# Kernel tuning notes

Hardware: AMD Instinct MI355X
Metric: run time of the kernel (lower is better)

## Reference

```python
import jax, jax.numpy as jnp
import numpy as np

B, L, D = 4, 2048, 1024
H = 16
HD = D // H  # head_dim = 64
BASE = 10000.0


def rope_cos_sin(seq_len, head_dim, dtype=jnp.float32):
    inv_freq = 1.0 / (BASE ** (jnp.arange(0, head_dim, 2, dtype=jnp.float32) / head_dim))
    t = jnp.arange(seq_len, dtype=jnp.float32)
    freqs = jnp.outer(t, inv_freq)  # [L, HD/2]
    return jnp.cos(freqs).astype(dtype), jnp.sin(freqs).astype(dtype)


def apply_rope(x, cos, sin):
    # x: [B, H, L, HD]; cos/sin: [L, HD/2]
    x1 = x[..., ::2]
    x2 = x[..., 1::2]
    c = cos[None, None, :, :]
    s = sin[None, None, :, :]
    # NOTE: original concatenates halves (does not re-interleave)
    return jnp.concatenate([x1 * c - x2 * s, x1 * s + x2 * c], axis=-1)


def setup_inputs() -> dict:
    key = jax.random.key(0)
    k1, k2, k3 = jax.random.split(key, 3)
    x = jax.random.normal(k1, (B, L, D), dtype=jnp.float32)
    W_qkv = jax.random.normal(k2, (3 * D, D), dtype=jnp.float32) * (D ** -0.5)
    W_proj = jax.random.normal(k3, (D, D), dtype=jnp.float32) * (D ** -0.5)
    return {"x": x, "W_qkv": W_qkv, "W_proj": W_proj}


def reference(x, W_qkv, W_proj):
    b, l, d = x.shape
    scale = HD ** -0.5
    qkv = jnp.einsum('bld,ed->ble', x, W_qkv)            # [B, L, 3D]
    qkv = qkv.reshape(b, l, 3, H, HD)
    q, k, v = (jnp.transpose(qkv[:, :, i], (0, 2, 1, 3)) for i in range(3))  # [B,H,L,HD]
    cos, sin = rope_cos_sin(l, HD, x.dtype)
    q = apply_rope(q, cos, sin)
    k = apply_rope(k, cos, sin)
    attn = jnp.einsum('bhqd,bhkd->bhqk', q, k) * scale   # [B,H,L,L]
    attn = jax.nn.softmax(attn, axis=-1)
    out = jnp.einsum('bhqk,bhkd->bhqd', attn, v)         # [B,H,L,HD]
    out = jnp.transpose(out, (0, 2, 1, 3)).reshape(b, l, d)
    return jnp.einsum('bld,ed->ble', out, W_proj)
```

## Files before the change

### kernel.cpp

```cpp
#include <hip/hip_runtime.h>
#include <hip/hip_bf16.h>

typedef unsigned short u16;
typedef unsigned int u32;
typedef __attribute__((ext_vector_type(8))) short bf16x8;
typedef __attribute__((ext_vector_type(4))) float f32x4;
typedef __attribute__((ext_vector_type(2))) unsigned int u32x2;

#define NL 2048
#define NH 16

__device__ __forceinline__ float bf2f(u16 v) {
    union { float f; unsigned u; } x; x.u = ((unsigned)v) << 16; return x.f;
}
__device__ __forceinline__ u16 f2bf(float f) {
    union { __hip_bfloat16 h; u16 u; } x; x.h = __float2bfloat16(f); return x.u;
}
__device__ __forceinline__ u32 pk2(float a, float b) {
    union { float f; u32 u; } x, y; x.f = a; y.f = b;
    return ((x.u + 0x8000u) >> 16) | ((y.u + 0x8000u) & 0xffff0000u);
}
__device__ __forceinline__ u32 pkt(float lo, float hi) {
    union { float f; u32 u; } x, y; x.f = lo; y.f = hi;
    return __builtin_amdgcn_perm(y.u, x.u, 0x07060302u);
}
#if __has_builtin(__builtin_amdgcn_exp2f)
#define EXP2F(x) __builtin_amdgcn_exp2f(x)
#else
#define EXP2F(x) __expf((x) * 0.69314718056f)
#endif

__device__ __forceinline__ void quad_xchg(u32& a, u32& b) {
#if __has_builtin(__builtin_amdgcn_permlane32_swap) && __has_builtin(__builtin_amdgcn_permlane16_swap)
    u32x2 r0 = __builtin_amdgcn_permlane32_swap(a, b, false, false);
    u32x2 r1 = __builtin_amdgcn_permlane16_swap(r0.x, r0.y, false, false);
    a = r1.x; b = r1.y;
#else
    asm volatile("s_nop 1\n\t"
                 "v_permlane32_swap_b32 %0, %1\n\t"
                 "s_nop 1\n\t"
                 "v_permlane16_swap_b32 %0, %1\n\t"
                 "s_nop 1"
                 : "+v"(a), "+v"(b));
#endif
}

__device__ __forceinline__ void gload_lds16(const u16* g, u16* l) {
    __builtin_amdgcn_global_load_lds(
        (__attribute__((address_space(1))) void*)(g),
        (__attribute__((address_space(3))) void*)(l), 16, 0, 0);
}

__global__ __launch_bounds__(256) void cast_all_k(const float* __restrict__ x,
                                                  const float* __restrict__ wq,
                                                  const float* __restrict__ wp,
                                                  u16* __restrict__ xo,
                                                  u16* __restrict__ wqo,
                                                  u16* __restrict__ wpo,
                                                  float* __restrict__ cosT,
                                                  float* __restrict__ sinT) {
    if (blockIdx.x < 256) {
        int idx = blockIdx.x * 256 + threadIdx.x;
        int l = idx >> 5, i = idx & 31;
        float invf = exp2f(-(float)i * 0.41524101186092029f);
        float ang = (float)l * invf;
        cosT[idx] = cosf(ang);
        sinT[idx] = sinf(ang);
    }
    int i = blockIdx.x * 256 + threadIdx.x;
    const float* src; u16* dst; int off;
    if (i < 2097152)      { src = x;  dst = xo;  off = i; }
    else if (i < 2883584) { src = wq; dst = wqo; off = i - 2097152; }
    else                  { src = wp; dst = wpo; off = i - 2883584; }
    float4 v = *(const float4*)&src[(size_t)off * 4];
    u16 tmp[4] = {f2bf(v.x), f2bf(v.y), f2bf(v.z), f2bf(v.w)};
    *(ushort4*)&dst[(size_t)off * 4] = *(ushort4*)tmp;
}

template <typename OutT>
__global__ __launch_bounds__(256) void gemm_bt(const u16* __restrict__ A,
                                               const u16* __restrict__ Bm,
                                               OutT* __restrict__ C,
                                               int M, int N, int K) {
    __shared__ u16 As[128][64];
    __shared__ u16 Bs[128][64];
    const int t = threadIdx.x;
    const int lane = t & 63, wave = t >> 6;
    const int quad = lane >> 4, lrow = lane & 15;
    const int wr = wave >> 1, wc = wave & 1;
    const size_t m0 = (size_t)blockIdx.y * 128, n0 = (size_t)blockIdx.x * 128;

    const int srow = wave * 32 + (lane >> 3);
    const int scg  = (lane & 7) ^ (lane >> 3);

    f32x4 acc[4][4];
#pragma unroll
    for (int i = 0; i < 4; ++i)
#pragma unroll
        for (int j = 0; j < 4; ++j) acc[i][j] = (f32x4)0.0f;

    for (int k0 = 0; k0 < K; k0 += 64) {
#pragma unroll
        for (int j = 0; j < 4; ++j) {
            gload_lds16(&A[(m0 + srow + j * 8) * K + k0 + scg * 8],
                        &As[wave * 32 + j * 8][0]);
            gload_lds16(&Bm[(n0 + srow + j * 8) * K + k0 + scg * 8],
                        &Bs[wave * 32 + j * 8][0]);
        }
        __syncthreads();
#pragma unroll
        for (int ks = 0; ks < 2; ++ks) {
            bf16x8 av[4], bv[4];
#pragma unroll
            for (int i = 0; i < 4; ++i)
                av[i] = *(const bf16x8*)
                    &As[wr * 64 + i * 16 + lrow][(((ks << 2) | quad) ^ (lrow & 7)) << 3];
#pragma unroll
            for (int j = 0; j < 4; ++j)
                bv[j] = *(const bf16x8*)
                    &Bs[wc * 64 + j * 16 + lrow][(((ks << 2) | quad) ^ (lrow & 7)) << 3];
#pragma unroll
            for (int i = 0; i < 4; ++i)
#pragma unroll
                for (int j = 0; j < 4; ++j)
                    acc[i][j] = __builtin_amdgcn_mfma_f32_16x16x32_bf16(
                        av[i], bv[j], acc[i][j], 0, 0, 0);
        }
        __syncthreads();
    }
#pragma unroll
    for (int i = 0; i < 4; ++i)
#pragma unroll
        for (int r = 0; r < 4; ++r) {
            size_t row = m0 + wr * 64 + i * 16 + quad * 4 + r;
#pragma unroll
            for (int j = 0; j < 4; ++j) {
                size_t col = n0 + wc * 64 + j * 16 + lrow;
                if constexpr (sizeof(OutT) == 4)
                    C[row * N + col] = acc[i][j][r];
                else
                    C[row * N + col] = f2bf(acc[i][j][r]);
            }
        }
}

__global__ __launch_bounds__(512, 2) void gemm256_bt(const u16* __restrict__ A,
                                                     const u16* __restrict__ Bm,
                                                     u16* __restrict__ C,
                                                     int M, int N, int K) {
    __shared__ __align__(16) char smem[131072];
    const int t = threadIdx.x;
    const int lane = t & 63, w = t >> 6;
    const int quad = lane >> 4, lq = lane & 15;
    const int wm = w >> 2, wn = w & 3;
    const int rsub = lane >> 3;
    const int scg  = (lane & 7) ^ rsub;
    const size_t m0 = (size_t)blockIdx.y * 256, n0 = (size_t)blockIdx.x * 256;
    const int NT = K >> 6;

#define ASB(buf) ((u16(*)[64])(smem + (size_t)(buf) * 65536))
#define BSB(buf) ((u16(*)[64])(smem + (size_t)(buf) * 65536 + 32768))
#define STAGE_A(buf, half, kt) { \
    const size_t kro_ = (size_t)(kt) * 64 + (size_t)(scg * 8); \
    gload_lds16(&A[(m0 + (half) * 128 + w * 16 + 0 + rsub) * (size_t)K + kro_], \
                &ASB(buf)[(half) * 128 + w * 16 + 0][0]); \
    gload_lds16(&A[(m0 + (half) * 128 + w * 16 + 8 + rsub) * (size_t)K + kro_], \
                &ASB(buf)[(half) * 128 + w * 16 + 8][0]); }
#define STAGE_B(buf, half, kt) { \
    const size_t kro_ = (size_t)(kt) * 64 + (size_t)(scg * 8); \
    gload_lds16(&Bm[(n0 + (half) * 128 + w * 16 + 0 + rsub) * (size_t)K + kro_], \
                &BSB(buf)[(half) * 128 + w * 16 + 0][0]); \
    gload_lds16(&Bm[(n0 + (half) * 128 + w * 16 + 8 + rsub) * (size_t)K + kro_], \
                &BSB(buf)[(half) * 128 + w * 16 + 8][0]); }
#define RD_A(dst, rowbase) { \
    _Pragma("unroll") for (int m_ = 0; m_ < 4; ++m_) \
    _Pragma("unroll") for (int ks_ = 0; ks_ < 2; ++ks_) \
        dst[m_][ks_] = *(const bf16x8*) \
            &Ac[(rowbase) + m_ * 16 + lq][(((ks_ << 2) | quad) ^ (lq & 7)) << 3]; }
#define RD_B(dst, rowbase) { \
    _Pragma("unroll") for (int n_ = 0; n_ < 2; ++n_) \
    _Pragma("unroll") for (int ks_ = 0; ks_ < 2; ++ks_) \
        dst[n_][ks_] = *(const bf16x8*) \
            &Bc[(rowbase) + n_ * 16 + lq][(((ks_ << 2) | quad) ^ (lq & 7)) << 3]; }
#define MM(QM, QN, bvv) { \
    _Pragma("unroll") for (int m_ = 0; m_ < 4; ++m_) \
    _Pragma("unroll") for (int n_ = 0; n_ < 2; ++n_) \
    _Pragma("unroll") for (int ks_ = 0; ks_ < 2; ++ks_) \
        acc[QM][QN][m_][n_] = __builtin_amdgcn_mfma_f32_16x16x32_bf16( \
            av[m_][ks_], bvv[n_][ks_], acc[QM][QN][m_][n_], 0, 0, 0); }

    f32x4 acc[2][2][4][2];
#pragma unroll
    for (int a = 0; a < 2; ++a)
#pragma unroll
        for (int b = 0; b < 2; ++b)
#pragma unroll
            for (int m = 0; m < 4; ++m)
#pragma unroll
                for (int n = 0; n < 2; ++n) acc[a][b][m][n] = (f32x4)0.0f;
    bf16x8 av[4][2], bv0[2][2], bv1[2][2];

    STAGE_A(0, 0, 0); STAGE_B(0, 0, 0); STAGE_B(0, 1, 0); STAGE_A(0, 1, 0);
    asm volatile("s_waitcnt vmcnt(4)" ::: "memory");
    __builtin_amdgcn_s_barrier();

    for (int kt = 0; kt < NT - 1; ++kt) {
        const int cur = kt & 1, nxt = cur ^ 1;
        u16 (*Ac)[64] = ASB(cur);
        u16 (*Bc)[64] = BSB(cur);

        RD_A(av, wm * 64);
        RD_B(bv0, wn * 32);
        STAGE_A(nxt, 0, kt + 1);
        __builtin_amdgcn_s_barrier();
        __builtin_amdgcn_s_setprio(1);
        MM(0, 0, bv0);
        __builtin_amdgcn_s_setprio(0);
        asm volatile("s_waitcnt vmcnt(4)" ::: "memory");
        __builtin_amdgcn_s_barrier();

        RD_B(bv1, 128 + wn * 32);
        STAGE_B(nxt, 0, kt + 1);
        __builtin_amdgcn_s_barrier();
        __builtin_amdgcn_s_setprio(1);
        MM(0, 1, bv1);
        __builtin_amdgcn_s_setprio(0);
        asm volatile("s_waitcnt vmcnt(4)" ::: "memory");
        __builtin_amdgcn_s_barrier();

        RD_A(av, 128 + wm * 64);
        STAGE_B(nxt, 1, kt + 1);
        __builtin_amdgcn_s_barrier();
        __builtin_amdgcn_s_setprio(1);
        MM(1, 1, bv1);
        __builtin_amdgcn_s_setprio(0);
        __builtin_amdgcn_s_barrier();

        RD_B(bv0, wn * 32);
        STAGE_A(nxt, 1, kt + 1);
        __builtin_amdgcn_s_barrier();
        __builtin_amdgcn_s_setprio(1);
        MM(1, 0, bv0);
        __builtin_amdgcn_s_setprio(0);
        asm volatile("s_waitcnt vmcnt(4)" ::: "memory");
        __builtin_amdgcn_s_barrier();
    }

    {
        u16 (*Ac)[64] = ASB((NT - 1) & 1);
        u16 (*Bc)[64] = BSB((NT - 1) & 1);
        RD_A(av, wm * 64);
        RD_B(bv0, wn * 32);
        MM(0, 0, bv0);
        asm volatile("s_waitcnt vmcnt(2)" ::: "memory");
        __builtin_amdgcn_s_barrier();
        RD_B(bv1, 128 + wn * 32);
        MM(0, 1, bv1);
        asm volatile("s_waitcnt vmcnt(0)" ::: "memory");
        __builtin_amdgcn_s_barrier();
        RD_A(av, 128 + wm * 64);
        MM(1, 1, bv1);
        MM(1, 0, bv0);
    }

#pragma unroll
    for (int QM = 0; QM < 2; ++QM)
#pragma unroll
        for (int QN = 0; QN < 2; ++QN)
#pragma unroll
            for (int m = 0; m < 4; ++m)
#pragma unroll
                for (int r = 0; r < 4; ++r) {
                    size_t row = m0 + QM * 128 + wm * 64 + m * 16 + quad * 4 + r;
#pragma unroll
                    for (int n = 0; n < 2; ++n) {
                        size_t col = n0 + QN * 128 + wn * 32 + n * 16 + lq;
                        C[row * N + col] = f2bf(acc[QM][QN][m][n][r]);
                    }
                }
#undef ASB
#undef BSB
#undef STAGE_A
#undef STAGE_B
#undef RD_A
#undef RD_B
#undef MM
}

__global__ __launch_bounds__(256) void rope_vt_k(const u16* __restrict__ qkv,
                                                 const float* __restrict__ cosT,
                                                 const float* __restrict__ sinT,
                                                 u16* __restrict__ Q,
                                                 u16* __restrict__ Ko,
                                                 u16* __restrict__ VT) {
    __shared__ u16 vtile[64][72];
    const int lt = blockIdx.x, bh = blockIdx.y;
    const int b = bh >> 4, h = bh & 15;
    const int l0 = lt * 64;
    const int t = threadIdx.x;
    const float SC = 0.180336879f;
#pragma unroll
    for (int c = 0; c < 2; ++c) {
        int flat8 = c * 256 + t;
        int li = flat8 >> 3, dg = flat8 & 7;
        const u16* rowp = qkv + (size_t)(b * NL + l0 + li) * 3072 + h * 64 + dg * 8;
        uint4 qv = *(const uint4*)rowp;
        uint4 kv = *(const uint4*)(rowp + 1024);
        uint4 vv = *(const uint4*)(rowp + 2048);
        *(uint4*)&vtile[li][dg * 8] = vv;
        float4 cs = *(const float4*)&cosT[(l0 + li) * 32 + dg * 4];
        float4 sn = *(const float4*)&sinT[(l0 + li) * 32 + dg * 4];
        union { float f; u32 u; } w;
        float e0, o0, e1, o1, e2, o2, e3, o3;
        w.u = qv.x << 16; e0 = w.f; w.u = qv.x & 0xffff0000u; o0 = w.f;
        w.u = qv.y << 16; e1 = w.f; w.u = qv.y & 0xffff0000u; o1 = w.f;
        w.u = qv.z << 16; e2 = w.f; w.u = qv.z & 0xffff0000u; o2 = w.f;
        w.u = qv.w << 16; e3 = w.f; w.u = qv.w & 0xffff0000u; o3 = w.f;
        float c0 = cs.x * SC, c1 = cs.y * SC, c2 = cs.z * SC, c3 = cs.w * SC;
        float s0 = sn.x * SC, s1 = sn.y * SC, s2 = sn.z * SC, s3 = sn.w * SC;
        size_t ob = ((size_t)(b * NH + h) * NL + l0 + li) * 64;
        *(uint2*)&Q[ob + dg * 4] =
            make_uint2(pk2(e0 * c0 - o0 * s0, e1 * c1 - o1 * s1),
                       pk2(e2 * c2 - o2 * s2, e3 * c3 - o3 * s3));
        *(uint2*)&Q[ob + 32 + dg * 4] =
            make_uint2(pk2(e0 * s0 + o0 * c0, e1 * s1 + o1 * c1),
                       pk2(e2 * s2 + o2 * c2, e3 * s3 + o3 * c3));
        float f0, g0, f1, g1, f2, g2, f3, g3;
        w.u = kv.x << 16; f0 = w.f; w.u = kv.x & 0xffff0000u; g0 = w.f;
        w.u = kv.y << 16; f1 = w.f; w.u = kv.y & 0xffff0000u; g1 = w.f;
        w.u = kv.z << 16; f2 = w.f; w.u = kv.z & 0xffff0000u; g2 = w.f;
        w.u = kv.w << 16; f3 = w.f; w.u = kv.w & 0xffff0000u; g3 = w.f;
        *(uint2*)&Ko[ob + dg * 4] =
            make_uint2(pk2(f0 * cs.x - g0 * sn.x, f1 * cs.y - g1 * sn.y),
                       pk2(f2 * cs.z - g2 * sn.z, f3 * cs.w - g3 * sn.w));
        *(uint2*)&Ko[ob + 32 + dg * 4] =
            make_uint2(pk2(f0 * sn.x + g0 * cs.x, f1 * sn.y + g1 * cs.y),
                       pk2(f2 * sn.z + g2 * cs.z, f3 * sn.w + g3 * cs.w));
    }
    __syncthreads();
#pragma unroll
    for (int c = 0; c < 2; ++c) {
        int flat8 = c * 256 + t;
        int d = flat8 >> 3, lg = flat8 & 7;
        u16 tmp[8];
#pragma unroll
        for (int e = 0; e < 8; ++e) tmp[e] = vtile[lg * 8 + e][d];
        *(uint4*)&VT[((size_t)(bh * 64 + d)) * NL + l0 + lg * 8] = *(uint4*)tmp;
    }
}

__global__ __launch_bounds__(512, 4) void attn_k(const u16* __restrict__ Q,
                                                 const u16* __restrict__ Kg,
                                                 const u16* __restrict__ VT,
                                                 u16* __restrict__ Og) {
    __shared__ __align__(16) char smem[65536];
    u16 (*KsB)[64][64] = (u16(*)[64][64])(smem);
    u16 (*VsB)[64][64] = (u16(*)[64][64])(smem + 16384);
    const int t = threadIdx.x;
    const int lane = t & 63, wave = t >> 6;
    const int quad = lane >> 4, lq = lane & 15;

    const int flat = blockIdx.y * 8 + blockIdx.x;
    const int qt = (flat >> 3) & 7;
    const int bh = (flat & 7) + ((flat >> 6) << 3);
    const int q0 = qt * 256;
    const size_t qkbase = (size_t)bh * NL * 64;

    const int rsub = lane >> 3;
    const int scg  = (lane & 7) ^ rsub;

    u16 (*Qtmp)[64] = (u16(*)[64])(smem + 32768);
#pragma unroll
    for (int j = 0; j < 4; ++j)
        gload_lds16(&Q[qkbase + (size_t)(q0 + wave * 32 + j * 8 + rsub) * 64 + scg * 8],
                    &Qtmp[wave * 32 + j * 8][0]);
    const u16* kptr = Kg + qkbase + (size_t)(wave * 8 + rsub) * 64 + scg * 8;
    const u16* vptr = VT + qkbase + (size_t)(wave * 8 + rsub) * NL + scg * 8;
    gload_lds16(kptr, &KsB[0][wave * 8][0]);
    gload_lds16(vptr, &VsB[0][wave * 8][0]);
    kptr += 64 * 64;
    vptr += 64;
    __syncthreads();
    bf16x8 bq[2][2];
#pragma unroll
    for (int qh = 0; qh < 2; ++qh)
#pragma unroll
        for (int ks = 0; ks < 2; ++ks)
            bq[qh][ks] = *(const bf16x8*)
                &Qtmp[wave * 32 + qh * 16 + lq][(((ks << 2) | quad) ^ (lq & 7)) << 3];

    const bf16x8 ones = (bf16x8)(short)16256;
    f32x4 ot[2][4];
#pragma unroll
    for (int qh = 0; qh < 2; ++qh)
#pragma unroll
        for (int mt = 0; mt < 4; ++mt) ot[qh][mt] = (f32x4)0.0f;
    f32x4 lacc[2] = {(f32x4)0.0f, (f32x4)0.0f};

    for (int kc = 0; kc < NL / 64; ++kc) {
        __syncthreads();
        if (kc < NL / 64 - 1) {
            gload_lds16(kptr, &KsB[(kc + 1) & 1][wave * 8][0]);
            gload_lds16(vptr, &VsB[(kc + 1) & 1][wave * 8][0]);
            kptr += 64 * 64;
            vptr += 64;
        }
        const int cur = kc & 1;

        f32x4 st[2][4];
#pragma unroll
        for (int qh = 0; qh < 2; ++qh)
#pragma unroll
            for (int mt = 0; mt < 4; ++mt) st[qh][mt] = (f32x4)0.0f;
#pragma unroll
        for (int half = 0; half < 2; ++half)
#pragma unroll
            for (int ks = 0; ks < 2; ++ks)
#pragma unroll
                for (int m2 = 0; m2 < 2; ++m2) {
                    const int mt = half * 2 + m2;
                    bf16x8 ak = *(const bf16x8*)
                        &KsB[cur][mt * 16 + lq][(((ks << 2) | quad) ^ (lq & 7)) << 3];
                    st[0][mt] = __builtin_amdgcn_mfma_f32_16x16x32_bf16(ak, bq[0][ks], st[0][mt], 0, 0, 0);
                    st[1][mt] = __builtin_amdgcn_mfma_f32_16x16x32_bf16(ak, bq[1][ks], st[1][mt], 0, 0, 0);
                }

#pragma unroll
        for (int ks = 0; ks < 2; ++ks) {
            bf16x8 av[4];
#pragma unroll
            for (int mt = 0; mt < 4; ++mt)
                av[mt] = *(const bf16x8*)
                    &VsB[cur][mt * 16 + lq][(((ks << 2) | quad) ^ (lq & 7)) << 3];

            bf16x8 bp[2];
#pragma unroll
            for (int qh = 0; qh < 2; ++qh) {
                u32 a0, b0, a1, b1;
                {
                    const int mt = 2 * ks;
                    a0 = pkt(EXP2F(st[qh][mt][0]), EXP2F(st[qh][mt][1]));
                    a1 = pkt(EXP2F(st[qh][mt][2]), EXP2F(st[qh][mt][3]));
                }
                {
                    const int mt = 2 * ks + 1;
                    b0 = pkt(EXP2F(st[qh][mt][0]), EXP2F(st[qh][mt][1]));
                    b1 = pkt(EXP2F(st[qh][mt][2]), EXP2F(st[qh][mt][3]));
                }
                quad_xchg(a0, b0);
                quad_xchg(a1, b1);
                union { u32 u[4]; bf16x8 v; } bb;
                bb.u[0] = a0;
                bb.u[1] = a1;
                bb.u[2] = b0;
                bb.u[3] = b1;
                bp[qh] = bb.v;
            }

            lacc[0] = __builtin_amdgcn_mfma_f32_16x16x32_bf16(ones, bp[0], lacc[0], 0, 0, 0);
            lacc[1] = __builtin_amdgcn_mfma_f32_16x16x32_bf16(ones, bp[1], lacc[1], 0, 0, 0);
#pragma unroll
            for (int mt = 0; mt < 4; ++mt) {
                ot[0][mt] = __builtin_amdgcn_mfma_f32_16x16x32_bf16(av[mt], bp[0], ot[0][mt], 0, 0, 0);
                ot[1][mt] = __builtin_amdgcn_mfma_f32_16x16x32_bf16(av[mt], bp[1], ot[1][mt], 0, 0, 0);
            }
        }
    }

    __syncthreads();
    float* OT_ls = (float*)(smem + wave * 4352);
    float* Ls_ls = (float*)(smem + 34816);
    const int b = bh >> 4, h = bh & 15;
    const int qq = lane >> 2, dblk = lane & 3;
#pragma unroll
    for (int qh = 0; qh < 2; ++qh) {
#pragma unroll
        for (int mt = 0; mt < 4; ++mt)
#pragma unroll
            for (int r = 0; r < 4; ++r)
                OT_ls[(mt * 16 + quad * 4 + r) * 17 + lq] = ot[qh][mt][r];
        if (quad == 0) Ls_ls[wave * 16 + lq] = lacc[qh][0];
        __builtin_amdgcn_s_waitcnt(0xc07f);

        float rls = 1.0f / Ls_ls[wave * 16 + qq];
        u16 tmp[16];
#pragma unroll
        for (int e = 0; e < 16; ++e)
            tmp[e] = f2bf(OT_ls[(dblk * 16 + e) * 17 + qq] * rls);
        size_t orow = (size_t)b * NL + q0 + wave * 32 + qh * 16 + qq;
        size_t obase = orow * 1024 + h * 64 + dblk * 16;
        *(uint4*)&Og[obase] = *(uint4*)&tmp[0];
        *(uint4*)&Og[obase + 8] = *(uint4*)&tmp[8];
    }
}

extern "C" void kernel_launch(void* const* d_in, const int* in_sizes, int n_in,
                              void* d_out, int out_size, void* d_ws, size_t ws_size,
                              hipStream_t stream) {
    const float* x     = (const float*)d_in[0];
    const float* Wqkv  = (const float*)d_in[1];
    const float* Wproj = (const float*)d_in[2];
    float* out = (float*)d_out;

    char* ws = (char*)d_ws;
    u16* qkv     = (u16*)ws;
    u16* attnout = (u16*)ws;
    u16* Qw      = (u16*)(ws + 50331648);
    u16* Kw      = (u16*)(ws + 67108864);
    u16* VTw     = (u16*)(ws + 83886080);
    float* cosT  = (float*)(ws + 100663296);
    float* sinT  = (float*)(ws + 100925440);
    u16* x_bf    = (u16*)(ws + 101187584);
    u16* Wqkv_bf = (u16*)(ws + 117964800);
    u16* Wproj_bf= (u16*)(ws + 124256256);

    cast_all_k<<<12288, 256, 0, stream>>>(x, Wqkv, Wproj, x_bf, Wqkv_bf, Wproj_bf,
                                          cosT, sinT);
    gemm256_bt<<<dim3(12, 32), 512, 0, stream>>>(x_bf, Wqkv_bf, qkv, 8192, 3072, 1024);
    rope_vt_k<<<dim3(32, 64), 256, 0, stream>>>(qkv, cosT, sinT, Qw, Kw, VTw);
    attn_k<<<dim3(8, 64), 512, 0, stream>>>(Qw, Kw, VTw, attnout);
    gemm_bt<float><<<dim3(8, 64), 256, 0, stream>>>(attnout, Wproj_bf, out, 8192, 1024, 1024);
}
```

Baseline: 270.1 us.

## Fuse RoPE, scaling and V transpose into the QKV GEMM epilogue

The QKV projection GEMM now writes Q and K directly in head-major layout with RoPE and the softmax scale applied, and writes V transposed. Neighbouring even/odd columns are paired with a lane shuffle. This removes the separate rope_vt_k kernel and the round trip of the bf16 qkv intermediate through global memory. In exchange the epilogue does scattered 2-byte stores with per-element cos/sin loads, which may coalesce poorly, and the cos/sin tables are packed into one float2 table.

```diff
diff --git a/kernel.cpp b/kernel.cpp
--- a/kernel.cpp
+++ b/kernel.cpp
@@ -10,15 +10,8 @@
 #define NL 2048
 #define NH 16
 
-__device__ __forceinline__ float bf2f(u16 v) {
-    union { float f; unsigned u; } x; x.u = ((unsigned)v) << 16; return x.f;
-}
 __device__ __forceinline__ u16 f2bf(float f) {
     union { __hip_bfloat16 h; u16 u; } x; x.h = __float2bfloat16(f); return x.u;
-}
-__device__ __forceinline__ u32 pk2(float a, float b) {
-    union { float f; u32 u; } x, y; x.f = a; y.f = b;
-    return ((x.u + 0x8000u) >> 16) | ((y.u + 0x8000u) & 0xffff0000u);
 }
 __device__ __forceinline__ u32 pkt(float lo, float hi) {
     union { float f; u32 u; } x, y; x.f = lo; y.f = hi;
@@ -57,15 +50,13 @@
                                                   u16* __restrict__ xo,
                                                   u16* __restrict__ wqo,
                                                   u16* __restrict__ wpo,
-                                                  float* __restrict__ cosT,
-                                                  float* __restrict__ sinT) {
+                                                  float2* __restrict__ cs2T) {
     if (blockIdx.x < 256) {
         int idx = blockIdx.x * 256 + threadIdx.x;
         int l = idx >> 5, i = idx & 31;
         float invf = exp2f(-(float)i * 0.41524101186092029f);
         float ang = (float)l * invf;
-        cosT[idx] = cosf(ang);
-        sinT[idx] = sinf(ang);
+        cs2T[idx] = make_float2(cosf(ang), sinf(ang));
     }
     int i = blockIdx.x * 256 + threadIdx.x;
     const float* src; u16* dst; int off;
@@ -144,10 +135,13 @@
         }
 }
 
-__global__ __launch_bounds__(512, 2) void gemm256_bt(const u16* __restrict__ A,
-                                                     const u16* __restrict__ Bm,
-                                                     u16* __restrict__ C,
-                                                     int M, int N, int K) {
+__global__ __launch_bounds__(512, 2) void gemm256_qkv(const u16* __restrict__ A,
+                                                      const u16* __restrict__ Bm,
+                                                      u16* __restrict__ Qo,
+                                                      u16* __restrict__ Ko,
+                                                      u16* __restrict__ VTo,
+                                                      const float2* __restrict__ cs2T,
+                                                      int M, int K) {
     __shared__ __align__(16) char smem[131072];
     const int t = threadIdx.x;
     const int lane = t & 63, w = t >> 6;
@@ -263,21 +257,64 @@
         MM(1, 0, bv0);
     }
 
-#pragma unroll
-    for (int QM = 0; QM < 2; ++QM)
+    const int sect = (int)(n0 >> 10);
+    const int colb = (int)(n0 & 1023);
+    if (sect < 2) {
+        u16* __restrict__ outp = sect ? Ko : Qo;
+        const float sc = sect ? 1.0f : 0.180336879f;
+        const int odd = lq & 1;
 #pragma unroll
         for (int QN = 0; QN < 2; ++QN)
 #pragma unroll
-            for (int m = 0; m < 4; ++m)
-#pragma unroll
-                for (int r = 0; r < 4; ++r) {
-                    size_t row = m0 + QM * 128 + wm * 64 + m * 16 + quad * 4 + r;
-#pragma unroll
-                    for (int n = 0; n < 2; ++n) {
-                        size_t col = n0 + QN * 128 + wn * 32 + n * 16 + lq;
-                        C[row * N + col] = f2bf(acc[QM][QN][m][n][r]);
+            for (int n = 0; n < 2; ++n) {
+                const int col = colb + QN * 128 + wn * 32 + n * 16 + lq;
+                const int h = col >> 6;
+                const int d2 = (col & 63) >> 1;
+                const int dim = d2 + 32 * odd;
+#pragma unroll
+                for (int QM = 0; QM < 2; ++QM)
+#pragma unroll
+                    for (int m = 0; m < 4; ++m) {
+                        const size_t row = m0 + QM * 128 + wm * 64 + m * 16 + quad * 4;
+                        const int l0 = (int)(row & 2047);
+                        const int b = (int)(row >> 11);
+                        const size_t ob = ((size_t)(b * 16 + h) * 2048 + l0) * 64 + dim;
+#pragma unroll
+                        for (int r = 0; r < 4; ++r) {
+                            float v = acc[QM][QN][m][n][r];
+                            float pv = __shfl_xor(v, 1, 64);
+                            float2 cs = cs2T[(l0 + r) * 32 + d2];
+                            float c = cs.x * sc, s = cs.y * sc;
+                            float outv = odd ? (pv * s + v * c)
+                                             : (v * c - pv * s);
+                            outp[ob + (size_t)r * 64] = f2bf(outv);
+                        }
                     }
-                }
+            }
+    } else {
+#pragma unroll
+        for (int QN = 0; QN < 2; ++QN)
+#pragma unroll
+            for (int n = 0; n < 2; ++n) {
+                const int col = colb + QN * 128 + wn * 32 + n * 16 + lq;
+                const int h = col >> 6;
+                const int d = col & 63;
+#pragma unroll
+                for (int QM = 0; QM < 2; ++QM)
+#pragma unroll
+                    for (int m = 0; m < 4; ++m) {
+                        const size_t row = m0 + QM * 128 + wm * 64 + m * 16 + quad * 4;
+                        const int l0 = (int)(row & 2047);
+                        const int b = (int)(row >> 11);
+                        u16 t4[4];
+#pragma unroll
+                        for (int r = 0; r < 4; ++r)
+                            t4[r] = f2bf(acc[QM][QN][m][n][r]);
+                        *(uint2*)&VTo[((size_t)((b * 16 + h) * 64 + d)) * 2048 + l0] =
+                            *(uint2*)t4;
+                    }
+            }
+    }
 #undef ASB
 #undef BSB
 #undef STAGE_A
@@ -285,68 +322,6 @@
 #undef RD_A
 #undef RD_B
 #undef MM
-}
-
-__global__ __launch_bounds__(256) void rope_vt_k(const u16* __restrict__ qkv,
-                                                 const float* __restrict__ cosT,
-                                                 const float* __restrict__ sinT,
-                                                 u16* __restrict__ Q,
-                                                 u16* __restrict__ Ko,
-                                                 u16* __restrict__ VT) {
-    __shared__ u16 vtile[64][72];
-    const int lt = blockIdx.x, bh = blockIdx.y;
-    const int b = bh >> 4, h = bh & 15;
-    const int l0 = lt * 64;
-    const int t = threadIdx.x;
-    const float SC = 0.180336879f;
-#pragma unroll
-    for (int c = 0; c < 2; ++c) {
-        int flat8 = c * 256 + t;
-        int li = flat8 >> 3, dg = flat8 & 7;
-        const u16* rowp = qkv + (size_t)(b * NL + l0 + li) * 3072 + h * 64 + dg * 8;
-        uint4 qv = *(const uint4*)rowp;
-        uint4 kv = *(const uint4*)(rowp + 1024);
-        uint4 vv = *(const uint4*)(rowp + 2048);
-        *(uint4*)&vtile[li][dg * 8] = vv;
-        float4 cs = *(const float4*)&cosT[(l0 + li) * 32 + dg * 4];
-        float4 sn = *(const float4*)&sinT[(l0 + li) * 32 + dg * 4];
-        union { float f; u32 u; } w;
-        float e0, o0, e1, o1, e2, o2, e3, o3;
-        w.u = qv.x << 16; e0 = w.f; w.u = qv.x & 0xffff0000u; o0 = w.f;
-        w.u = qv.y << 16; e1 = w.f; w.u = qv.y & 0xffff0000u; o1 = w.f;
-        w.u = qv.z << 16; e2 = w.f; w.u = qv.z & 0xffff0000u; o2 = w.f;
-        w.u = qv.w << 16; e3 = w.f; w.u = qv.w & 0xffff0000u; o3 = w.f;
-        float c0 = cs.x * SC, c1 = cs.y * SC, c2 = cs.z * SC, c3 = cs.w * SC;
-        float s0 = sn.x * SC, s1 = sn.y * SC, s2 = sn.z * SC, s3 = sn.w * SC;
-        size_t ob = ((size_t)(b * NH + h) * NL + l0 + li) * 64;
-        *(uint2*)&Q[ob + dg * 4] =
-            make_uint2(pk2(e0 * c0 - o0 * s0, e1 * c1 - o1 * s1),
-                       pk2(e2 * c2 - o2 * s2, e3 * c3 - o3 * s3));
-        *(uint2*)&Q[ob + 32 + dg * 4] =
-            make_uint2(pk2(e0 * s0 + o0 * c0, e1 * s1 + o1 * c1),
-                       pk2(e2 * s2 + o2 * c2, e3 * s3 + o3 * c3));
-        float f0, g0, f1, g1, f2, g2, f3, g3;
-        w.u = kv.x << 16; f0 = w.f; w.u = kv.x & 0xffff0000u; g0 = w.f;
-        w.u = kv.y << 16; f1 = w.f; w.u = kv.y & 0xffff0000u; g1 = w.f;
-        w.u = kv.z << 16; f2 = w.f; w.u = kv.z & 0xffff0000u; g2 = w.f;
-        w.u = kv.w << 16; f3 = w.f; w.u = kv.w & 0xffff0000u; g3 = w.f;
-        *(uint2*)&Ko[ob + dg * 4] =
-            make_uint2(pk2(f0 * cs.x - g0 * sn.x, f1 * cs.y - g1 * sn.y),
-                       pk2(f2 * cs.z - g2 * sn.z, f3 * cs.w - g3 * sn.w));
-        *(uint2*)&Ko[ob + 32 + dg * 4] =
-            make_uint2(pk2(f0 * sn.x + g0 * cs.x, f1 * sn.y + g1 * cs.y),
-                       pk2(f2 * sn.z + g2 * cs.z, f3 * sn.w + g3 * cs.w));
-    }
-    __syncthreads();
-#pragma unroll
-    for (int c = 0; c < 2; ++c) {
-        int flat8 = c * 256 + t;
-        int d = flat8 >> 3, lg = flat8 & 7;
-        u16 tmp[8];
-#pragma unroll
-        for (int e = 0; e < 8; ++e) tmp[e] = vtile[lg * 8 + e][d];
-        *(uint4*)&VT[((size_t)(bh * 64 + d)) * NL + l0 + lg * 8] = *(uint4*)tmp;
-    }
 }
 
 __global__ __launch_bounds__(512, 4) void attn_k(const u16* __restrict__ Q,
@@ -503,21 +478,19 @@
     float* out = (float*)d_out;
 
     char* ws = (char*)d_ws;
-    u16* qkv     = (u16*)ws;
     u16* attnout = (u16*)ws;
     u16* Qw      = (u16*)(ws + 50331648);
     u16* Kw      = (u16*)(ws + 67108864);
     u16* VTw     = (u16*)(ws + 83886080);
-    float* cosT  = (float*)(ws + 100663296);
-    float* sinT  = (float*)(ws + 100925440);
+    float2* cs2T = (float2*)(ws + 100663296);
     u16* x_bf    = (u16*)(ws + 101187584);
     u16* Wqkv_bf = (u16*)(ws + 117964800);
     u16* Wproj_bf= (u16*)(ws + 124256256);
 
     cast_all_k<<<12288, 256, 0, stream>>>(x, Wqkv, Wproj, x_bf, Wqkv_bf, Wproj_bf,
-                                          cosT, sinT);
-    gemm256_bt<<<dim3(12, 32), 512, 0, stream>>>(x_bf, Wqkv_bf, qkv, 8192, 3072, 1024);
-    rope_vt_k<<<dim3(32, 64), 256, 0, stream>>>(qkv, cosT, sinT, Qw, Kw, VTw);
+                                          cs2T);
+    gemm256_qkv<<<dim3(12, 32), 512, 0, stream>>>(x_bf, Wqkv_bf, Qw, Kw, VTw,
+                                                  cs2T, 8192, 1024);
     attn_k<<<dim3(8, 64), 512, 0, stream>>>(Qw, Kw, VTw, attnout);
     gemm_bt<float><<<dim3(8, 64), 256, 0, stream>>>(attnout, Wproj_bf, out, 8192, 1024, 1024);
 }
```

After: 284.0 us. 1.05x slower.
